# Kernel optimization log

Hardware: AMD Instinct MI355X
Metric: run time of the kernel (lower is better)

## Reference

```python
import jax, jax.numpy as jnp
import numpy as np
import math

N_HEAD = 16

def setup_inputs() -> dict:
    key = jax.random.key(0)
    ks = jax.random.split(key, 5)
    B, T, C = 4, 2048, 2048
    s = 1.0 / math.sqrt(C)
    return {
        "x": jax.random.normal(ks[0], (B, T, C), jnp.float32),
        "w_attn": jax.random.normal(ks[1], (C, 3 * C), jnp.float32) * s,
        "b_attn": jax.random.normal(ks[2], (3 * C,), jnp.float32) * 0.01,
        "w_proj": jax.random.normal(ks[3], (C, C), jnp.float32) * s,
        "b_proj": jax.random.normal(ks[4], (C,), jnp.float32) * 0.01,
    }

def reference(x, w_attn, b_attn, w_proj, b_proj):
    B, T, C = x.shape
    H = N_HEAD
    D = C // H
    # fused QKV projection: [B,T,3C] -> [3,B,H,T,D]
    qkv = (x @ w_attn + b_attn).reshape(B, T, 3, H, D).transpose(2, 0, 3, 1, 4)
    q, k, v = qkv[0], qkv[1], qkv[2]
    scale = 1.0 / math.sqrt(D)
    scores = jnp.einsum("bhqd,bhkd->bhqk", q, k) * scale  # [B,H,T,T]
    causal = jnp.tril(jnp.ones((T, T), dtype=bool))
    neg = jnp.finfo(scores.dtype).min
    scores = jnp.where(causal, scores, neg)
    attn = jax.nn.softmax(scores, axis=-1)
    y = jnp.einsum("bhqk,bhkd->bhqd", attn, v)  # [B,H,T,D]
    y = y.transpose(0, 2, 1, 3).reshape(B, T, C)
    return y @ w_proj + b_proj
```

## Files before the change

kernel.cpp:

```cpp
#include <hip/hip_runtime.h>
#include <hip/hip_bf16.h>
#include <stdint.h>

typedef unsigned short u16;
typedef __bf16 bf16x8 __attribute__((ext_vector_type(8)));
typedef unsigned short u16x8 __attribute__((ext_vector_type(8)));
typedef float f32x4 __attribute__((ext_vector_type(4)));
typedef float f32x16 __attribute__((ext_vector_type(16)));

__device__ __forceinline__ float bf2f(u16 u){ union{float f; unsigned i;} v; v.i = ((unsigned)u)<<16; return v.f; }
__device__ __forceinline__ u16 f2bf(float f){ union{float f; unsigned i;} v; v.f=f; unsigned r = v.i + 0x7FFFu + ((v.i>>16)&1u); return (u16)(r>>16); }

__device__ __forceinline__ void async16(const void* g, void* l){
  __builtin_amdgcn_global_load_lds((const __attribute__((address_space(1))) void*)g,
                                   (__attribute__((address_space(3))) void*)l, 16, 0, 0);
}

__global__ __launch_bounds__(256) void cvt_f2b(const float* __restrict__ src, u16* __restrict__ dst, int n)
{
  int i = (blockIdx.x * 256 + threadIdx.x) * 4;
  if (i < n) {
    float4 v = *(const float4*)&src[i];
    ushort4 o;
    o.x = f2bf(v.x); o.y = f2bf(v.y); o.z = f2bf(v.z); o.w = f2bf(v.w);
    *(ushort4*)&dst[i] = o;
  }
}

__global__ __launch_bounds__(256) void transpose2d_f2b(const float* __restrict__ src, u16* __restrict__ dst,
                                                       int src_rows, int src_cols)
{
  __shared__ u16 tile[64][72];
  const int r0 = blockIdx.y << 6, c0 = blockIdx.x << 6;
  const int t = threadIdx.x;
  #pragma unroll
  for (int i=0;i<4;i++){
    int slot = t + (i<<8);
    int r = slot >> 4, cv = (slot & 15) << 2;
    float4 v = *(const float4*)&src[(size_t)(r0+r)*src_cols + c0 + cv];
    tile[r][cv+0] = f2bf(v.x); tile[r][cv+1] = f2bf(v.y);
    tile[r][cv+2] = f2bf(v.z); tile[r][cv+3] = f2bf(v.w);
  }
  __syncthreads();
  #pragma unroll
  for (int i=0;i<2;i++){
    int slot = t + (i<<8);
    int cr = slot >> 3, rv = (slot & 7) << 3;
    u16x8 v;
    #pragma unroll
    for (int e=0;e<8;e++) v[e] = tile[rv+e][cr];
    *(u16x8*)&dst[(size_t)(c0+cr)*src_rows + r0 + rv] = v;
  }
}

__global__ __launch_bounds__(256) void transpose_v(const u16* __restrict__ qkv, u16* __restrict__ vt)
{
  __shared__ u16 tile[64][72];
  const int bh = blockIdx.z;
  const int b = bh >> 4, h = bh & 15;
  const u16* src = qkv + (size_t)b*2048*6144 + 4096 + h*128;
  u16* dst = vt + (size_t)bh*128*2048;
  const int t0 = blockIdx.y << 6, d0 = blockIdx.x << 6;
  const int t = threadIdx.x;
  #pragma unroll
  for (int i=0;i<2;i++){
    int slot = t + (i<<8);
    int r = slot >> 3, cv = (slot & 7) << 3;
    *(u16x8*)&tile[r][cv] = *(const u16x8*)&src[(size_t)(t0+r)*6144 + d0 + cv];
  }
  __syncthreads();
  #pragma unroll
  for (int i=0;i<2;i++){
    int slot = t + (i<<8);
    int cr = slot >> 3, rv = (slot & 7) << 3;
    u16x8 v;
    #pragma unroll
    for (int e=0;e<8;e++) v[e] = tile[rv+e][cr];
    *(u16x8*)&dst[(size_t)(d0+cr)*2048 + t0 + rv] = v;
  }
}

template<int F32OUT>
__global__ __launch_bounds__(512, 2) void gemm8p(const u16* __restrict__ A, const u16* __restrict__ Bt,
                                                 const float* __restrict__ bias, void* __restrict__ Cv,
                                                 int M, int N, int K, int ntn)
{
  __shared__ u16 lsA[2][2][256*32];
  __shared__ u16 lsB[2][2][256*32];
  const int tid = threadIdx.x;
  const int w = tid >> 6, lane = tid & 63;
  const int wm = w >> 2, wn = w & 3;
  const int l5 = lane >> 5, l31 = lane & 31;

  const int nwg = gridDim.x;
  const int bid = blockIdx.x;
  const int swz = (bid & 7) * (nwg >> 3) + (bid >> 3);
  const int nt = swz % ntn, mt = swz / ntn;
  const int m0 = mt << 8, n0 = nt << 8;
  const int NT = K >> 6, NI = NT >> 1;

  const int s0 = tid, s1 = tid + 512;
  const size_t off0 = (size_t)(s0>>2)*K + (size_t)((((s0&3) ^ ((s0>>3)&3))) << 3);
  const size_t off1 = (size_t)(s1>>2)*K + (size_t)((((s1&3) ^ ((s1>>3)&3))) << 3);
  const u16* Asrc = A + (size_t)m0*K;
  const u16* Bsrc = Bt + (size_t)n0*K;

  f32x16 acc[4][2];
  #pragma unroll
  for (int i=0;i<4;i++)
    #pragma unroll
    for (int j=0;j<2;j++)
      #pragma unroll
      for (int e=0;e<16;e++) acc[i][j][e] = 0.f;

  bf16x8 aE[4], aO[4], bX[4], bY[4];

#define SLOT(T, KH, AP, BP) do { \
    const u16* as_ = Asrc + (T)*64 + (KH)*32; \
    const u16* bs_ = Bsrc + (T)*64 + (KH)*32; \
    async16(as_ + off0, &(AP)[s0*8]); \
    async16(as_ + off1, &(AP)[s1*8]); \
    async16(bs_ + off0, &(BP)[s0*8]); \
    async16(bs_ + off1, &(BP)[s1*8]); \
  } while(0)

#define RDA(SET, BUF, KS, Q) do { \
    _Pragma("unroll") \
    for (int mb=0; mb<2; ++mb){ \
      int row_ = wm*128 + (Q)*64 + mb*32 + l31; \
      _Pragma("unroll") \
      for (int ks=0; ks<2; ++ks){ \
        int g_ = (ks*2 + l5) ^ ((row_>>1) & 3); \
        SET[mb*2+ks] = *(const bf16x8*)&lsA[BUF][KS][row_*32 + (g_<<3)]; \
      } \
    } } while(0)

#define RDB(SET, BUF, KS) do { \
    _Pragma("unroll") \
    for (int nb=0; nb<2; ++nb){ \
      int row_ = wn*64 + nb*32 + l31; \
      _Pragma("unroll") \
      for (int ks=0; ks<2; ++ks){ \
        int g_ = (ks*2 + l5) ^ ((row_>>1) & 3); \
        SET[nb*2+ks] = *(const bf16x8*)&lsB[BUF][KS][row_*32 + (g_<<3)]; \
      } \
    } } while(0)

#define MM(Q, AS, BS) do { \
    __builtin_amdgcn_s_setprio(1); \
    _Pragma("unroll") \
    for (int mb=0; mb<2; ++mb) \
      _Pragma("unroll") \
      for (int nb=0; nb<2; ++nb) \
        _Pragma("unroll") \
        for (int ks=0; ks<2; ++ks) \
          acc[(Q)*2+mb][nb] = __builtin_amdgcn_mfma_f32_32x32x16_bf16(AS[mb*2+ks], BS[nb*2+ks], acc[(Q)*2+mb][nb], 0,0,0); \
    __builtin_amdgcn_s_setprio(0); \
  } while(0)

#define LGK4 do { asm volatile("s_waitcnt lgkmcnt(4)" ::: "memory"); __builtin_amdgcn_sched_barrier(0); } while(0)
#define LGK8 do { asm volatile("s_waitcnt lgkmcnt(8)" ::: "memory"); __builtin_amdgcn_sched_barrier(0); } while(0)
#define LGK0 do { asm volatile("s_waitcnt lgkmcnt(0)" ::: "memory"); __builtin_amdgcn_sched_barrier(0); } while(0)
#define VM8 asm volatile("s_waitcnt vmcnt(8)" ::: "memory")
#define VM4 asm volatile("s_waitcnt vmcnt(4)" ::: "memory")
#define VM0 asm volatile("s_waitcnt vmcnt(0)" ::: "memory")
#define ENDP do { __builtin_amdgcn_s_barrier(); __builtin_amdgcn_sched_barrier(0); } while(0)

  SLOT(0, 0, lsA[0][0], lsB[0][0]);
  SLOT(0, 1, lsA[0][1], lsB[0][1]);
  SLOT(1, 0, lsA[1][0], lsB[1][0]);
  VM8;
  __builtin_amdgcn_s_barrier();
  __builtin_amdgcn_sched_barrier(0);
  RDA(aO, 0,0, 0); RDB(bX, 0,0);

  #pragma unroll 1
  for (int i = 0; i < NI-1; ++i){
    const int t0 = 2*i;
    RDA(aE, 0,0, 1); SLOT(t0+1,1, lsA[1][1], lsB[1][1]); LGK4; MM(0, aO, bX); VM8; ENDP;
    RDA(aO, 0,1, 0); RDB(bY, 0,1);                       LGK8; MM(1, aE, bX);      ENDP;
    RDA(aE, 0,1, 1); SLOT(t0+2,0, lsA[0][0], lsB[0][0]); LGK4; MM(0, aO, bY); VM8; ENDP;
    RDA(aO, 1,0, 0); RDB(bX, 1,0);                       LGK8; MM(1, aE, bY);      ENDP;
    RDA(aE, 1,0, 1); SLOT(t0+2,1, lsA[0][1], lsB[0][1]); LGK4; MM(0, aO, bX); VM8; ENDP;
    RDA(aO, 1,1, 0); RDB(bY, 1,1);                       LGK8; MM(1, aE, bX);      ENDP;
    RDA(aE, 1,1, 1); SLOT(t0+3,0, lsA[1][0], lsB[1][0]); LGK4; MM(0, aO, bY); VM8; ENDP;
    RDA(aO, 0,0, 0); RDB(bX, 0,0);                       LGK8; MM(1, aE, bY);      ENDP;
  }
  RDA(aE, 0,0, 1); SLOT(NT-1,1, lsA[1][1], lsB[1][1]);   LGK4; MM(0, aO, bX); VM8; ENDP;
  RDA(aO, 0,1, 0); RDB(bY, 0,1);                         LGK8; MM(1, aE, bX);      ENDP;
  RDA(aE, 0,1, 1);                                       LGK4; MM(0, aO, bY); VM4; ENDP;
  RDA(aO, 1,0, 0); RDB(bX, 1,0);                         LGK8; MM(1, aE, bY);      ENDP;
  RDA(aE, 1,0, 1);                                       LGK4; MM(0, aO, bX); VM0; ENDP;
  RDA(aO, 1,1, 0); RDB(bY, 1,1);                         LGK8; MM(1, aE, bX);      ENDP;
  RDA(aE, 1,1, 1);                                       LGK4; MM(0, aO, bY);      ENDP;
                                                         LGK0; MM(1, aE, bY);

#undef SLOT
#undef RDA
#undef RDB
#undef MM

  float bv[2];
  #pragma unroll
  for (int nb=0;nb<2;nb++) bv[nb] = bias[n0 + wn*64 + nb*32 + l31];
  #pragma unroll
  for (int am=0;am<4;am++){
    #pragma unroll
    for (int nb=0;nb<2;nb++){
      int col = n0 + wn*64 + nb*32 + l31;
      #pragma unroll
      for (int r=0;r<16;r++){
        int row = m0 + wm*128 + am*32 + (r&3) + 8*(r>>2) + 4*l5;
        float vv = acc[am][nb][r] + bv[nb];
        if (F32OUT) ((float*)Cv)[(size_t)row*N + col] = vv;
        else        ((u16*)Cv)[(size_t)row*N + col] = f2bf(vv);
      }
    }
  }
}

__global__ __launch_bounds__(512, 4) void attn_fwd(const u16* __restrict__ qkv, const u16* __restrict__ vt,
                                                   u16* __restrict__ y)
{
  __shared__ u16 kb[2][64*128];
  __shared__ u16 vb[2][128*64];
  __shared__ u16 plds[8][16*64];
  const int bh = blockIdx.y;
  const int b = bh >> 4, h = bh & 15;
  const int pair = blockIdx.x;
  const int tid = threadIdx.x;
  const int w = tid >> 6, lane = tid & 63;
  const int lo = lane & 15, hi = lane >> 4;

  const u16* Qb = qkv + (size_t)b*2048*6144 + h*128;
  const u16* Kb = Qb + 2048;
  const u16* Vb = vt + (size_t)bh*128*2048;
  u16* pw = &plds[w][0];
  const float sc = 0.08838834764831845f * 1.4426950408889634f;
  f32x4 z = {0.f,0.f,0.f,0.f};

  #pragma unroll 1
  for (int seg = 0; seg < 2; ++seg){
    const int qt = seg ? pair : 15 - pair;
    const int qw = qt*128 + w*16;
    const int nt = qt*2 + 2;

    bf16x8 qf[4];
    #pragma unroll
    for (int kd=0;kd<4;kd++)
      qf[kd] = *(const bf16x8*)&Qb[(size_t)(qw + lo)*6144 + kd*32 + hi*8];

    f32x4 o[8];
    #pragma unroll
    for (int dj=0;dj<8;dj++) o[dj] = z;
    float mx[4], lsum[4];
    #pragma unroll
    for (int r=0;r<4;r++){ mx[r] = -3.0e38f; lsum[r] = 0.f; }

    #pragma unroll
    for (int i=0;i<2;i++){
      int slot = i*512 + tid;
      int kr = slot >> 4;
      int kc = ((slot & 15) << 4) ^ ((kr & 7) << 4);
      async16(Kb + (size_t)kr*6144 + (kc >> 1), &kb[0][(size_t)(i*512 + w*64)*8]);
      int vr = slot >> 3;
      int vc = ((slot & 7) << 4) ^ ((vr & 7) << 4);
      async16(Vb + (size_t)vr*2048 + (vc >> 1), &vb[0][(size_t)(i*512 + w*64)*8]);
    }
    __syncthreads();

    #pragma unroll 1
    for (int it = 0; it < nt; ++it){
      const int k0 = it*64;
      if (it + 1 < nt){
        const int kn = (it+1)*64;
        u16* kdst = kb[(it+1)&1];
        u16* vdst = vb[(it+1)&1];
        #pragma unroll
        for (int i=0;i<2;i++){
          int slot = i*512 + tid;
          int kr = slot >> 4;
          int kc = ((slot & 15) << 4) ^ ((kr & 7) << 4);
          async16(Kb + (size_t)(kn + kr)*6144 + (kc >> 1), &kdst[(size_t)(i*512 + w*64)*8]);
          int vr = slot >> 3;
          int vc = ((slot & 7) << 4) ^ ((vr & 7) << 4);
          async16(Vb + (size_t)vr*2048 + kn + (vc >> 1), &vdst[(size_t)(i*512 + w*64)*8]);
        }
      }
      if (k0 <= qw + 15){
        const u16* kcur = kb[it&1];
        const u16* vcur = vb[it&1];
        f32x4 s[4];
        #pragma unroll
        for (int t=0;t<4;t++) s[t] = z;
        __builtin_amdgcn_s_setprio(1);
        #pragma unroll
        for (int t=0;t<4;t++){
          #pragma unroll
          for (int kd=0;kd<4;kd++){
            int row = t*16 + lo;
            int cb = (kd*64 + hi*16) ^ ((lo & 7) << 4);
            bf16x8 kk = *(const bf16x8*)&kcur[row*128 + (cb >> 1)];
            s[t] = __builtin_amdgcn_mfma_f32_16x16x32_bf16(qf[kd], kk, s[t], 0,0,0);
          }
        }
        __builtin_amdgcn_s_setprio(0);

        if (k0 + 63 > qw) {
          #pragma unroll
          for (int t=0;t<4;t++)
            #pragma unroll
            for (int r=0;r<4;r++){
              int q = qw + hi*4 + r;
              int k = k0 + t*16 + lo;
              if (k > q) s[t][r] = -3.0e38f;
            }
        }
        #pragma unroll
        for (int r=0;r<4;r++){
          float tm = fmaxf(fmaxf(s[0][r], s[1][r]), fmaxf(s[2][r], s[3][r]));
          tm = fmaxf(tm, __shfl_xor(tm, 1));
          tm = fmaxf(tm, __shfl_xor(tm, 2));
          tm = fmaxf(tm, __shfl_xor(tm, 4));
          tm = fmaxf(tm, __shfl_xor(tm, 8));
          tm *= sc;
          float mn = fmaxf(mx[r], tm);
          float al = exp2f(mx[r] - mn);
          mx[r] = mn;
          float p0 = exp2f(fmaf(s[0][r], sc, -mn));
          float p1 = exp2f(fmaf(s[1][r], sc, -mn));
          float p2 = exp2f(fmaf(s[2][r], sc, -mn));
          float p3 = exp2f(fmaf(s[3][r], sc, -mn));
          float sum = (p0 + p1) + (p2 + p3);
          sum += __shfl_xor(sum, 1);
          sum += __shfl_xor(sum, 2);
          sum += __shfl_xor(sum, 4);
          sum += __shfl_xor(sum, 8);
          lsum[r] = lsum[r]*al + sum;
          #pragma unroll
          for (int dj=0;dj<8;dj++) o[dj][r] *= al;
          int row = hi*4 + r;
          int sw = (row & 7) << 4;
          u16* prow = pw + row*64;
          prow[((     lo*2) ^ sw) >> 1] = f2bf(p0);
          prow[((32 + lo*2) ^ sw) >> 1] = f2bf(p1);
          prow[((64 + lo*2) ^ sw) >> 1] = f2bf(p2);
          prow[((96 + lo*2) ^ sw) >> 1] = f2bf(p3);
        }

        bf16x8 pa[2];
        #pragma unroll
        for (int kf=0;kf<2;kf++)
          pa[kf] = *(const bf16x8*)&pw[(lo*128 + ((kf*64 + hi*16) ^ ((lo & 7) << 4))) >> 1];
        __builtin_amdgcn_s_setprio(1);
        #pragma unroll
        for (int dj=0;dj<8;dj++){
          int row = dj*16 + lo;
          int cb0 = (hi*16)      ^ ((lo & 7) << 4);
          int cb1 = (64 + hi*16) ^ ((lo & 7) << 4);
          bf16x8 vv0 = *(const bf16x8*)&vcur[row*64 + (cb0 >> 1)];
          bf16x8 vv1 = *(const bf16x8*)&vcur[row*64 + (cb1 >> 1)];
          o[dj] = __builtin_amdgcn_mfma_f32_16x16x32_bf16(pa[0], vv0, o[dj], 0,0,0);
          o[dj] = __builtin_amdgcn_mfma_f32_16x16x32_bf16(pa[1], vv1, o[dj], 0,0,0);
        }
        __builtin_amdgcn_s_setprio(0);
      }
      __syncthreads();
    }

    #pragma unroll
    for (int r=0;r<4;r++){
      float inv = 1.0f / lsum[r];
      size_t row = (size_t)(b*2048 + qw + hi*4 + r);
      #pragma unroll
      for (int dj=0;dj<8;dj++)
        y[row*2048 + h*128 + dj*16 + lo] = f2bf(o[dj][r] * inv);
    }
    __syncthreads();
  }
}

extern "C" void kernel_launch(void* const* d_in, const int* in_sizes, int n_in,
                              void* d_out, int out_size, void* d_ws, size_t ws_size,
                              hipStream_t stream) {
  (void)in_sizes; (void)n_in; (void)out_size; (void)ws_size;
  const float* x      = (const float*)d_in[0];
  const float* w_attn = (const float*)d_in[1];
  const float* b_attn = (const float*)d_in[2];
  const float* w_proj = (const float*)d_in[3];
  const float* b_proj = (const float*)d_in[4];
  float* out = (float*)d_out;

  char* ws = (char*)d_ws;
  u16* xbf = (u16*)(ws);
  u16* wT  = (u16*)(ws + 33554432);
  u16* pT  = (u16*)(ws + 58720256);
  u16* qkv = (u16*)(ws + 67108864);
  u16* vt  = (u16*)(ws + 167772160);
  u16* y   = xbf;

  cvt_f2b<<<16384, 256, 0, stream>>>(x, xbf, 8192*2048);
  transpose2d_f2b<<<dim3(96,32), 256, 0, stream>>>(w_attn, wT, 2048, 6144);
  transpose2d_f2b<<<dim3(32,32), 256, 0, stream>>>(w_proj, pT, 2048, 2048);
  gemm8p<0><<<768, 512, 0, stream>>>(xbf, wT, b_attn, qkv, 8192, 6144, 2048, 24);
  transpose_v<<<dim3(2,32,64), 256, 0, stream>>>(qkv, vt);
  attn_fwd<<<dim3(8,64), 512, 0, stream>>>(qkv, vt, y);
  gemm8p<1><<<256, 512, 0, stream>>>(y, pT, b_proj, out, 8192, 2048, 2048, 8);
}
```

Measured before the change: 512.5 us.

## Give each attention wave 32 query rows, register-staged K/V prefetch and lazy rescale

The attention kernel now runs 4 waves of 256 threads per block instead of 8. Each wave handles 32 query rows (two 16-row fragments), so every K and V fragment read from LDS feeds twice as many MFMAs. The double-buffered async global-to-LDS loads are replaced by a single LDS buffer, with the next tile prefetched into registers and written to LDS after a barrier. The online softmax also skips the running-max update and the output rescale when no row's max grows by more than 8 in log2 units. The costs are higher register pressure, an extra barrier per tile, and less latency hiding because there are fewer waves per block.

```diff
diff --git a/kernel.cpp b/kernel.cpp
--- a/kernel.cpp
+++ b/kernel.cpp
@@ -219,12 +219,12 @@
   }
 }
 
-__global__ __launch_bounds__(512, 4) void attn_fwd(const u16* __restrict__ qkv, const u16* __restrict__ vt,
+__global__ __launch_bounds__(256, 2) void attn_fwd(const u16* __restrict__ qkv, const u16* __restrict__ vt,
                                                    u16* __restrict__ y)
 {
-  __shared__ u16 kb[2][64*128];
-  __shared__ u16 vb[2][128*64];
-  __shared__ u16 plds[8][16*64];
+  __shared__ u16 kb[64*128];
+  __shared__ u16 vb[128*64];
+  __shared__ u16 plds[4][32*64];
   const int bh = blockIdx.y;
   const int b = bh >> 4, h = bh & 15;
   const int pair = blockIdx.x;
@@ -239,33 +239,53 @@
   const float sc = 0.08838834764831845f * 1.4426950408889634f;
   f32x4 z = {0.f,0.f,0.f,0.f};
 
+  size_t kgo[4], vgo[4];
+  int kof[4], vof[4];
+  #pragma unroll
+  for (int j=0;j<4;j++){
+    int i = tid + j*256;
+    int kr = i >> 4, kc = i & 15;
+    kgo[j] = (size_t)kr*6144 + kc*8;
+    kof[j] = kr*128 + ((((kc<<4) ^ ((kr&7)<<4))) >> 1);
+    int vr = i >> 3, vc = i & 7;
+    vgo[j] = (size_t)vr*2048 + vc*8;
+    vof[j] = vr*64 + ((((vc<<4) ^ ((vr&7)<<4))) >> 1);
+  }
+
   #pragma unroll 1
   for (int seg = 0; seg < 2; ++seg){
     const int qt = seg ? pair : 15 - pair;
-    const int qw = qt*128 + w*16;
+    const int qw = qt*128 + w*32;
     const int nt = qt*2 + 2;
 
-    bf16x8 qf[4];
-    #pragma unroll
-    for (int kd=0;kd<4;kd++)
-      qf[kd] = *(const bf16x8*)&Qb[(size_t)(qw + lo)*6144 + kd*32 + hi*8];
-
-    f32x4 o[8];
-    #pragma unroll
-    for (int dj=0;dj<8;dj++) o[dj] = z;
-    float mx[4], lsum[4];
-    #pragma unroll
-    for (int r=0;r<4;r++){ mx[r] = -3.0e38f; lsum[r] = 0.f; }
-
-    #pragma unroll
-    for (int i=0;i<2;i++){
-      int slot = i*512 + tid;
-      int kr = slot >> 4;
-      int kc = ((slot & 15) << 4) ^ ((kr & 7) << 4);
-      async16(Kb + (size_t)kr*6144 + (kc >> 1), &kb[0][(size_t)(i*512 + w*64)*8]);
-      int vr = slot >> 3;
-      int vc = ((slot & 7) << 4) ^ ((vr & 7) << 4);
-      async16(Vb + (size_t)vr*2048 + (vc >> 1), &vb[0][(size_t)(i*512 + w*64)*8]);
+    bf16x8 qf[2][4];
+    #pragma unroll
+    for (int f=0;f<2;f++)
+      #pragma unroll
+      for (int kd=0;kd<4;kd++)
+        qf[f][kd] = *(const bf16x8*)&Qb[(size_t)(qw + f*16 + lo)*6144 + kd*32 + hi*8];
+
+    f32x4 o[2][8];
+    #pragma unroll
+    for (int f=0;f<2;f++)
+      #pragma unroll
+      for (int dj=0;dj<8;dj++) o[f][dj] = z;
+    float mx[2][4], lsum[2][4];
+    #pragma unroll
+    for (int f=0;f<2;f++)
+      #pragma unroll
+      for (int r=0;r<4;r++){ mx[f][r] = -3.0e38f; lsum[f][r] = 0.f; }
+
+    uint4 krg[4], vrg[4];
+    #pragma unroll
+    for (int j=0;j<4;j++){
+      krg[j] = *(const uint4*)&Kb[kgo[j]];
+      vrg[j] = *(const uint4*)&Vb[vgo[j]];
+    }
+    #pragma unroll
+    for (int j=0;j<4;j++){
+      *(uint4*)&kb[kof[j]] = krg[j];
+      *(uint4*)&vb[vof[j]] = vrg[j];
     }
     __syncthreads();
 
@@ -273,110 +293,162 @@
     for (int it = 0; it < nt; ++it){
       const int k0 = it*64;
       if (it + 1 < nt){
-        const int kn = (it+1)*64;
-        u16* kdst = kb[(it+1)&1];
-        u16* vdst = vb[(it+1)&1];
-        #pragma unroll
-        for (int i=0;i<2;i++){
-          int slot = i*512 + tid;
-          int kr = slot >> 4;
-          int kc = ((slot & 15) << 4) ^ ((kr & 7) << 4);
-          async16(Kb + (size_t)(kn + kr)*6144 + (kc >> 1), &kdst[(size_t)(i*512 + w*64)*8]);
-          int vr = slot >> 3;
-          int vc = ((slot & 7) << 4) ^ ((vr & 7) << 4);
-          async16(Vb + (size_t)vr*2048 + kn + (vc >> 1), &vdst[(size_t)(i*512 + w*64)*8]);
+        const size_t knb = (size_t)(it+1)*64*6144;
+        const int vnb = (it+1)*64;
+        #pragma unroll
+        for (int j=0;j<4;j++){
+          krg[j] = *(const uint4*)&Kb[knb + kgo[j]];
+          vrg[j] = *(const uint4*)&Vb[vgo[j] + vnb];
         }
       }
-      if (k0 <= qw + 15){
-        const u16* kcur = kb[it&1];
-        const u16* vcur = vb[it&1];
-        f32x4 s[4];
-        #pragma unroll
-        for (int t=0;t<4;t++) s[t] = z;
+      if (k0 <= qw + 31){
+        f32x4 s[2][4];
+        #pragma unroll
+        for (int f=0;f<2;f++)
+          #pragma unroll
+          for (int t=0;t<4;t++) s[f][t] = z;
         __builtin_amdgcn_s_setprio(1);
         #pragma unroll
         for (int t=0;t<4;t++){
+          bf16x8 kk[4];
           #pragma unroll
           for (int kd=0;kd<4;kd++){
             int row = t*16 + lo;
             int cb = (kd*64 + hi*16) ^ ((lo & 7) << 4);
-            bf16x8 kk = *(const bf16x8*)&kcur[row*128 + (cb >> 1)];
-            s[t] = __builtin_amdgcn_mfma_f32_16x16x32_bf16(qf[kd], kk, s[t], 0,0,0);
+            kk[kd] = *(const bf16x8*)&kb[row*128 + (cb >> 1)];
           }
+          #pragma unroll
+          for (int f=0;f<2;f++)
+            #pragma unroll
+            for (int kd=0;kd<4;kd++)
+              s[f][t] = __builtin_amdgcn_mfma_f32_16x16x32_bf16(qf[f][kd], kk[kd], s[f][t], 0,0,0);
         }
         __builtin_amdgcn_s_setprio(0);
 
-        if (k0 + 63 > qw) {
-          #pragma unroll
-          for (int t=0;t<4;t++)
+        #pragma unroll
+        for (int f=0;f<2;f++){
+          if (k0 + 63 > qw + f*16) {
+            #pragma unroll
+            for (int t=0;t<4;t++)
+              #pragma unroll
+              for (int r=0;r<4;r++){
+                int q = qw + f*16 + hi*4 + r;
+                int k = k0 + t*16 + lo;
+                if (k > q) s[f][t][r] = -3.0e38f;
+              }
+          }
+        }
+        float tm[2][4];
+        int grow = 1;
+        #pragma unroll
+        for (int f=0;f<2;f++)
+          #pragma unroll
+          for (int r=0;r<4;r++){
+            float t0 = fmaxf(fmaxf(s[f][0][r], s[f][1][r]), fmaxf(s[f][2][r], s[f][3][r]));
+            t0 = fmaxf(t0, __shfl_xor(t0, 1));
+            t0 = fmaxf(t0, __shfl_xor(t0, 2));
+            t0 = fmaxf(t0, __shfl_xor(t0, 4));
+            t0 = fmaxf(t0, __shfl_xor(t0, 8));
+            tm[f][r] = t0 * sc;
+            grow &= (tm[f][r] <= mx[f][r] + 8.0f) ? 1 : 0;
+          }
+        if (__all(grow)) {
+          #pragma unroll
+          for (int f=0;f<2;f++)
             #pragma unroll
             for (int r=0;r<4;r++){
-              int q = qw + hi*4 + r;
-              int k = k0 + t*16 + lo;
-              if (k > q) s[t][r] = -3.0e38f;
+              float mn = mx[f][r];
+              float p0 = exp2f(fmaf(s[f][0][r], sc, -mn));
+              float p1 = exp2f(fmaf(s[f][1][r], sc, -mn));
+              float p2 = exp2f(fmaf(s[f][2][r], sc, -mn));
+              float p3 = exp2f(fmaf(s[f][3][r], sc, -mn));
+              float sum = (p0 + p1) + (p2 + p3);
+              sum += __shfl_xor(sum, 1);
+              sum += __shfl_xor(sum, 2);
+              sum += __shfl_xor(sum, 4);
+              sum += __shfl_xor(sum, 8);
+              lsum[f][r] += sum;
+              int row = f*16 + hi*4 + r;
+              int sw = (row & 7) << 4;
+              u16* prow = pw + row*64;
+              prow[((     lo*2) ^ sw) >> 1] = f2bf(p0);
+              prow[((32 + lo*2) ^ sw) >> 1] = f2bf(p1);
+              prow[((64 + lo*2) ^ sw) >> 1] = f2bf(p2);
+              prow[((96 + lo*2) ^ sw) >> 1] = f2bf(p3);
             }
-        }
-        #pragma unroll
-        for (int r=0;r<4;r++){
-          float tm = fmaxf(fmaxf(s[0][r], s[1][r]), fmaxf(s[2][r], s[3][r]));
-          tm = fmaxf(tm, __shfl_xor(tm, 1));
-          tm = fmaxf(tm, __shfl_xor(tm, 2));
-          tm = fmaxf(tm, __shfl_xor(tm, 4));
-          tm = fmaxf(tm, __shfl_xor(tm, 8));
-          tm *= sc;
-          float mn = fmaxf(mx[r], tm);
-          float al = exp2f(mx[r] - mn);
-          mx[r] = mn;
-          float p0 = exp2f(fmaf(s[0][r], sc, -mn));
-          float p1 = exp2f(fmaf(s[1][r], sc, -mn));
-          float p2 = exp2f(fmaf(s[2][r], sc, -mn));
-          float p3 = exp2f(fmaf(s[3][r], sc, -mn));
-          float sum = (p0 + p1) + (p2 + p3);
-          sum += __shfl_xor(sum, 1);
-          sum += __shfl_xor(sum, 2);
-          sum += __shfl_xor(sum, 4);
-          sum += __shfl_xor(sum, 8);
-          lsum[r] = lsum[r]*al + sum;
-          #pragma unroll
-          for (int dj=0;dj<8;dj++) o[dj][r] *= al;
-          int row = hi*4 + r;
-          int sw = (row & 7) << 4;
-          u16* prow = pw + row*64;
-          prow[((     lo*2) ^ sw) >> 1] = f2bf(p0);
-          prow[((32 + lo*2) ^ sw) >> 1] = f2bf(p1);
-          prow[((64 + lo*2) ^ sw) >> 1] = f2bf(p2);
-          prow[((96 + lo*2) ^ sw) >> 1] = f2bf(p3);
-        }
-
-        bf16x8 pa[2];
-        #pragma unroll
-        for (int kf=0;kf<2;kf++)
-          pa[kf] = *(const bf16x8*)&pw[(lo*128 + ((kf*64 + hi*16) ^ ((lo & 7) << 4))) >> 1];
+        } else {
+          #pragma unroll
+          for (int f=0;f<2;f++)
+            #pragma unroll
+            for (int r=0;r<4;r++){
+              float mn = fmaxf(mx[f][r], tm[f][r]);
+              float al = exp2f(mx[f][r] - mn);
+              mx[f][r] = mn;
+              float p0 = exp2f(fmaf(s[f][0][r], sc, -mn));
+              float p1 = exp2f(fmaf(s[f][1][r], sc, -mn));
+              float p2 = exp2f(fmaf(s[f][2][r], sc, -mn));
+              float p3 = exp2f(fmaf(s[f][3][r], sc, -mn));
+              float sum = (p0 + p1) + (p2 + p3);
+              sum += __shfl_xor(sum, 1);
+              sum += __shfl_xor(sum, 2);
+              sum += __shfl_xor(sum, 4);
+              sum += __shfl_xor(sum, 8);
+              lsum[f][r] = lsum[f][r]*al + sum;
+              #pragma unroll
+              for (int dj=0;dj<8;dj++) o[f][dj][r] *= al;
+              int row = f*16 + hi*4 + r;
+              int sw = (row & 7) << 4;
+              u16* prow = pw + row*64;
+              prow[((     lo*2) ^ sw) >> 1] = f2bf(p0);
+              prow[((32 + lo*2) ^ sw) >> 1] = f2bf(p1);
+              prow[((64 + lo*2) ^ sw) >> 1] = f2bf(p2);
+              prow[((96 + lo*2) ^ sw) >> 1] = f2bf(p3);
+            }
+        }
+
+        bf16x8 pa[2][2];
+        #pragma unroll
+        for (int f=0;f<2;f++)
+          #pragma unroll
+          for (int kf=0;kf<2;kf++)
+            pa[f][kf] = *(const bf16x8*)&pw[((f*16 + lo)*128 + ((kf*64 + hi*16) ^ ((lo & 7) << 4))) >> 1];
         __builtin_amdgcn_s_setprio(1);
         #pragma unroll
         for (int dj=0;dj<8;dj++){
           int row = dj*16 + lo;
           int cb0 = (hi*16)      ^ ((lo & 7) << 4);
           int cb1 = (64 + hi*16) ^ ((lo & 7) << 4);
-          bf16x8 vv0 = *(const bf16x8*)&vcur[row*64 + (cb0 >> 1)];
-          bf16x8 vv1 = *(const bf16x8*)&vcur[row*64 + (cb1 >> 1)];
-          o[dj] = __builtin_amdgcn_mfma_f32_16x16x32_bf16(pa[0], vv0, o[dj], 0,0,0);
-          o[dj] = __builtin_amdgcn_mfma_f32_16x16x32_bf16(pa[1], vv1, o[dj], 0,0,0);
+          bf16x8 vv0 = *(const bf16x8*)&vb[row*64 + (cb0 >> 1)];
+          bf16x8 vv1 = *(const bf16x8*)&vb[row*64 + (cb1 >> 1)];
+          #pragma unroll
+          for (int f=0;f<2;f++){
+            o[f][dj] = __builtin_amdgcn_mfma_f32_16x16x32_bf16(pa[f][0], vv0, o[f][dj], 0,0,0);
+            o[f][dj] = __builtin_amdgcn_mfma_f32_16x16x32_bf16(pa[f][1], vv1, o[f][dj], 0,0,0);
+          }
         }
         __builtin_amdgcn_s_setprio(0);
       }
       __syncthreads();
+      if (it + 1 < nt){
+        #pragma unroll
+        for (int j=0;j<4;j++){
+          *(uint4*)&kb[kof[j]] = krg[j];
+          *(uint4*)&vb[vof[j]] = vrg[j];
+        }
+      }
+      __syncthreads();
     }
 
     #pragma unroll
-    for (int r=0;r<4;r++){
-      float inv = 1.0f / lsum[r];
-      size_t row = (size_t)(b*2048 + qw + hi*4 + r);
-      #pragma unroll
-      for (int dj=0;dj<8;dj++)
-        y[row*2048 + h*128 + dj*16 + lo] = f2bf(o[dj][r] * inv);
-    }
-    __syncthreads();
+    for (int f=0;f<2;f++)
+      #pragma unroll
+      for (int r=0;r<4;r++){
+        float inv = 1.0f / lsum[f][r];
+        size_t row = (size_t)(b*2048 + qw + f*16 + hi*4 + r);
+        #pragma unroll
+        for (int dj=0;dj<8;dj++)
+          y[row*2048 + h*128 + dj*16 + lo] = f2bf(o[f][dj][r] * inv);
+      }
   }
 }
 
@@ -404,6 +476,6 @@
   transpose2d_f2b<<<dim3(32,32), 256, 0, stream>>>(w_proj, pT, 2048, 2048);
   gemm8p<0><<<768, 512, 0, stream>>>(xbf, wT, b_attn, qkv, 8192, 6144, 2048, 24);
   transpose_v<<<dim3(2,32,64), 256, 0, stream>>>(qkv, vt);
-  attn_fwd<<<dim3(8,64), 512, 0, stream>>>(qkv, vt, y);
+  attn_fwd<<<dim3(8,64), 256, 0, stream>>>(qkv, vt, y);
   gemm8p<1><<<256, 512, 0, stream>>>(y, pT, b_proj, out, 8192, 2048, 2048, 8);
 }
```

Result: slower. 993.8 us (+93.9%).
